# Performance work log

Measured on AMD Instinct MI355X. Metric: run time of the kernel, lower is better.

The kernel has to match this reference:

```python
import jax, jax.numpy as jnp
import numpy as np

NL = 30  # self.nl_size
EPS = 1e-5


def _conv(x, W, b, pad):
    # NCHW conv, OIHW weights
    y = jax.lax.conv_general_dilated(x, W, (1, 1), [(pad, pad), (pad, pad)],
                                     dimension_numbers=('NCHW', 'OIHW', 'NCHW'))
    return y + b[None, :, None, None]


def _gn1(x, g, b):
    # GroupNorm with 1 group: normalize over (C,H,W) per sample, per-channel affine
    mu = jnp.mean(x, axis=(1, 2, 3), keepdims=True)
    var = jnp.var(x, axis=(1, 2, 3), keepdims=True)
    return (x - mu) * jax.lax.rsqrt(var + EPS) * g[None, :, None, None] + b[None, :, None, None]


def _block(x, W, b, g, be):
    # up_conv: Conv3x3 -> GroupNorm(1) -> ReLU
    return jax.nn.relu(_gn1(_conv(x, W, b, 1), g, be))


def _resize(x, h, w):
    # matches F.interpolate(mode='bilinear', align_corners=False)
    return jax.image.resize(x, (x.shape[0], x.shape[1], h, w), method='bilinear')


def setup_inputs() -> dict:
    key = jax.random.key(0)
    ks = jax.random.split(key, 16)
    B, feat, H, W = 4, 64, 300, 300
    s = 0.05
    d = {}
    d['fdm'] = jax.random.normal(ks[0], (B, 1, H, W), jnp.float32)
    d['x0'] = jax.random.normal(ks[1], (B, 64, 300, 300), jnp.float32)
    d['x1'] = jax.random.normal(ks[2], (B, 64, 150, 150), jnp.float32)
    d['x2'] = jax.random.normal(ks[3], (B, 64, 75, 75), jnp.float32)
    d['x3'] = jax.random.normal(ks[4], (B, 64, 38, 38), jnp.float32)
    d['x4'] = jax.random.normal(ks[5], (B, 64, 19, 19), jnp.float32)
    # self.fuse: Conv2d(192, feat, 3) + GN(1, feat)
    d['fuse_W'] = jax.random.normal(ks[6], (feat, 192, 3, 3), jnp.float32) * s
    d['fuse_b'] = jnp.zeros((feat,), jnp.float32)
    d['fuse_g'] = jnp.ones((feat,), jnp.float32)
    d['fuse_be'] = jnp.zeros((feat,), jnp.float32)
    # self.bcg_conv: Conv2d(feat, 1, 1)
    d['bcg_W'] = jax.random.normal(ks[7], (1, feat, 1, 1), jnp.float32) * s
    d['bcg_b'] = jnp.zeros((1,), jnp.float32)
    # self.fuse0: Conv2d(feat, feat, 3) + GN(1, feat)
    d['fuse0_W'] = jax.random.normal(ks[8], (feat, feat, 3, 3), jnp.float32) * s
    d['fuse0_b'] = jnp.zeros((feat,), jnp.float32)
    d['fuse0_g'] = jnp.ones((feat,), jnp.float32)
    d['fuse0_be'] = jnp.zeros((feat,), jnp.float32)
    # self.sup: Conv2d(feat, 1, 1)
    d['sup_W'] = jax.random.normal(ks[9], (1, feat, 1, 1), jnp.float32) * s
    d['sup_b'] = jnp.zeros((1,), jnp.float32)
    return d


def reference(fdm, x0, x1, x2, x3, x4,
              fuse_W, fuse_b, fuse_g, fuse_be,
              bcg_W, bcg_b,
              fuse0_W, fuse0_b, fuse0_g, fuse0_be,
              sup_W, sup_b):
    H, W = fdm.shape[2], fdm.shape[3]
    # x0/x1 are interpolated in the original forward but never used downstream.
    x2r = _resize(x2, H, W)
    x3r = _resize(x3, H, W)
    x4r = _resize(x4, H, W)
    base = _block(jnp.concatenate([x2r, x3r, x4r], axis=1), fuse_W, fuse_b, fuse_g, fuse_be)
    bcg = jax.nn.sigmoid(_conv(base, bcg_W, bcg_b, 0))
    mean_bcg = jnp.mean(bcg, axis=(2, 3), keepdims=True)
    fdm_m = fdm * (bcg > mean_bcg).astype(fdm.dtype)
    nl_feat = _block(base, fuse0_W, fuse0_b, fuse0_g, fuse0_be)
    nl_feat = _resize(nl_feat, NL, NL)  # (b,c,30,30)
    b, c = nl_feat.shape[0], nl_feat.shape[1]
    kh, kw = H // NL, W // NL
    # adaptive_max_pool2d with divisible input: exact window max
    pooled = fdm_m.reshape(b, 1, NL, kh, NL, kw).max(axis=(3, 5))  # (b,1,30,30)
    nl_fdm = pooled * nl_feat  # (b,c,30,30)
    A = nl_fdm.reshape(b, c, NL * NL)   # (b,c,900)
    Bm = nl_feat.reshape(b, c, NL * NL)  # (b,c,900)
    # nl[b,i] = max_j sum_c A[b,c,i] * Bm[b,c,j]
    nl = jnp.max(jnp.einsum('bci,bcj->bij', A, Bm), axis=2)  # (b,900)
    fdm_exp = _resize(nl.reshape(b, 1, NL, NL), H, W)
    base2 = fdm_exp * base
    sup = _conv(base2, sup_W, sup_b, 0)
    return (fdm_m, bcg, base2, sup)
```

## Files before the change

### kernel.cpp

```cpp
#include <hip/hip_runtime.h>
#include <math.h>

typedef unsigned int uint;
typedef unsigned short ushort;
typedef __attribute__((ext_vector_type(8))) short bf16x8;
typedef __attribute__((ext_vector_type(8))) _Float16 f16x8;
typedef __attribute__((ext_vector_type(4))) float f32x4;

#define HWp 90000

__device__ __forceinline__ float bf2f(ushort u) { return __uint_as_float(((uint)u) << 16); }
__device__ __forceinline__ ushort f2bf(float f) {
    uint u = __float_as_uint(f);
    uint r = (u + 0x7FFFu + ((u >> 16) & 1u)) >> 16;
    return (ushort)r;
}
__device__ __forceinline__ ushort f2h(float f) { _Float16 h = (_Float16)f; ushort u; __builtin_memcpy(&u, &h, 2); return u; }
__device__ __forceinline__ float h2f(ushort u) { _Float16 h; __builtin_memcpy(&h, &u, 2); return (float)h; }
__device__ __forceinline__ uint enc(float f) {
    uint u = __float_as_uint(f);
    return (u & 0x80000000u) ? ~u : (u | 0x80000000u);
}
__device__ __forceinline__ float dec(uint k) {
    uint u = (k & 0x80000000u) ? (k ^ 0x80000000u) : ~k;
    return __uint_as_float(u);
}

__global__ __launch_bounds__(256) void k_repack_fsplit(const float* __restrict__ Wf, ushort* __restrict__ Ws) {
    int i = blockIdx.x * 256 + threadIdx.x;
    if (i >= 221184) return;
    int j = i & 7; int l = (i >> 3) & 63; int n = (i >> 9) & 3;
    int r = i >> 11; int tap = r % 9; int ck = (r / 9) % 6; int wsel = r / 54;
    int oc = n * 16 + (l & 15);
    int c  = ck * 32 + ((l >> 4) << 3) + j;
    float w = Wf[(size_t)oc * 1728 + c * 9 + tap] * 256.0f;
    ushort h = f2h(w);
    Ws[i] = wsel ? f2h(w - h2f(h)) : h;
}
__global__ __launch_bounds__(256) void k_repack_f0(const float* __restrict__ W0, ushort* __restrict__ Wfrag) {
    int i = blockIdx.x * 256 + threadIdx.x;
    if (i >= 36864) return;
    int j = i & 7; int l = (i >> 3) & 63; int octile = (i >> 9) & 3;
    int kstep = (i >> 11) & 1; int tap = i >> 12;
    int oc = octile * 16 + (l & 15);
    int c  = kstep * 32 + (l >> 4) * 8 + j;
    Wfrag[i] = f2bf(W0[(size_t)oc * 576 + c * 9 + tap]);
}

__global__ __launch_bounds__(256, 4) void k_fuse_mfma(
    const float* __restrict__ x2, const float* __restrict__ x3, const float* __restrict__ x4,
    const ushort* __restrict__ Ws, const float* __restrict__ bfv,
    float* __restrict__ preb, double* __restrict__ part)
{
    __shared__ char lds_a[108 * 144];
    __shared__ int   t_y0[18], t_y1[18];
    __shared__ float t_wy[18];
    __shared__ int   t_x0[54], t_x1[54];
    __shared__ float t_wx[54];
    __shared__ double red[8];
    const int tid = threadIdx.x;
    const int lane = tid & 63, w = tid >> 6;
    const int bz = blockIdx.z;
    const int y0 = blockIdx.y * 4;
    const int x0 = blockIdx.x * 16;
    const int mg = lane >> 4, mr = lane & 15;

    for (int i = tid; i < 72; i += 256) {
        int lev = i / 24, k = i - lev * 24;
        int n = (lev == 0) ? 75 : (lev == 1 ? 38 : 19);
        float scale = (float)n * (1.0f / 300.0f);
        if (k < 6) {
            int gy = y0 + k - 1;
            float fy = ((float)gy + 0.5f) * scale - 0.5f;
            float fl = floorf(fy); int iy = (int)fl; float ay = fy - fl;
            t_y0[lev * 6 + k] = min(max(iy, 0), n - 1) * n;
            t_y1[lev * 6 + k] = min(iy + 1, n - 1) * n;
            t_wy[lev * 6 + k] = ay;
        } else {
            int j = k - 6;
            int gx = x0 + j - 1;
            float fx = ((float)gx + 0.5f) * scale - 0.5f;
            float fl = floorf(fx); int ix = (int)fl; float ax = fx - fl;
            t_x0[lev * 18 + j] = min(max(ix, 0), n - 1);
            t_x1[lev * 18 + j] = min(ix + 1, n - 1);
            t_wx[lev * 18 + j] = ax;
        }
    }
    __syncthreads();

    f32x4 acc[4];
#pragma unroll
    for (int ot = 0; ot < 4; ++ot) acc[ot] = f32x4{0.f, 0.f, 0.f, 0.f};

    for (int ck = 0; ck < 6; ++ck) {
        const int lev = ck >> 1;
        const float* src = (lev == 0) ? x2 : (lev == 1 ? x3 : x4);
        const int n = (lev == 0) ? 75 : (lev == 1 ? 38 : 19);
        const float* plane0 = src + (size_t)(bz * 64 + (ck & 1) * 32) * n * n;
        for (int e = tid; e < 3456; e += 256) {
            int ch = e / 108;
            int px = e - ch * 108;
            int hy = px / 18, hx = px - hy * 18;
            int gy = y0 + hy - 1, gx = x0 + hx - 1;
            float a = 0.f;
            if ((uint)gy < 300u && (uint)gx < 300u) {
                const float* sp = plane0 + (size_t)ch * n * n;
                int r0 = t_y0[lev * 6 + hy], r1 = t_y1[lev * 6 + hy]; float fy = t_wy[lev * 6 + hy];
                int c0 = t_x0[lev * 18 + hx], c1 = t_x1[lev * 18 + hx]; float fx = t_wx[lev * 18 + hx];
                float v00 = sp[r0 + c0], v01 = sp[r0 + c1];
                float v10 = sp[r1 + c0], v11 = sp[r1 + c1];
                a = ((1.f - fy) * ((1.f - fx) * v00 + fx * v01)
                   + fy * ((1.f - fx) * v10 + fx * v11)) * 256.0f;
            }
            ushort hi = f2h(a);
            ushort lo = f2h(a - h2f(hi));
            char* p = lds_a + px * 144 + ch * 2;
            *(ushort*)p = hi;
            *(ushort*)(p + 64) = lo;
        }
        __syncthreads();
#pragma unroll
        for (int tap = 0; tap < 9; ++tap) {
            const int p = (w + tap / 3) * 18 + (mr + tap % 3);
            const char* ap = lds_a + p * 144 + mg * 16;
            f16x8 ah = *(const f16x8*)ap;
            f16x8 al = *(const f16x8*)(ap + 64);
            const ushort* wh = Ws + ((size_t)(ck * 9 + tap)) * 2048 + lane * 8;
            const ushort* wl = wh + 54 * 2048;
#pragma unroll
            for (int ot = 0; ot < 4; ++ot) {
                f16x8 bh = *(const f16x8*)(wh + ot * 512);
                acc[ot] = __builtin_amdgcn_mfma_f32_16x16x32_f16(ah, bh, acc[ot], 0, 0, 0);
                acc[ot] = __builtin_amdgcn_mfma_f32_16x16x32_f16(al, bh, acc[ot], 0, 0, 0);
                f16x8 bl = *(const f16x8*)(wl + ot * 512);
                acc[ot] = __builtin_amdgcn_mfma_f32_16x16x32_f16(ah, bl, acc[ot], 0, 0, 0);
            }
        }
        __syncthreads();
    }
    const int yo = y0 + w;
    float s = 0.f, ss = 0.f;
#pragma unroll
    for (int ot = 0; ot < 4; ++ot) {
        int oc = ot * 16 + mr;
        float bia = bfv[oc];
#pragma unroll
        for (int i2 = 0; i2 < 4; ++i2) {
            int xo = x0 + mg * 4 + i2;
            if (xo < 300) {
                float t = acc[ot][i2] * (1.0f / 65536.0f) + bia;
                preb[(size_t)(bz * 64 + oc) * HWp + yo * 300 + xo] = t;
                s += t; ss += t * t;
            }
        }
    }
    double ds = s, dss = ss;
    for (int off = 32; off; off >>= 1) { ds += __shfl_down(ds, off); dss += __shfl_down(dss, off); }
    if (lane == 0) { red[w * 2] = ds; red[w * 2 + 1] = dss; }
    __syncthreads();
    if (tid == 0) {
        double S = red[0] + red[2] + red[4] + red[6];
        double SS = red[1] + red[3] + red[5] + red[7];
        int blin = (bz * 75 + blockIdx.y) * 19 + blockIdx.x;
        part[2 * blin] = S; part[2 * blin + 1] = SS;
    }
}

__global__ __launch_bounds__(256, 4) void k_fuse0_conv(
    const float* __restrict__ basep, const ushort* __restrict__ Wfrag,
    const float* __restrict__ b0, ushort* __restrict__ f0c, double* __restrict__ part)
{
    __shared__ ushort lds_x[108 * 64];
    __shared__ double red[8];
    const int tid = threadIdx.x;
    const int lane = tid & 63, w = tid >> 6;
    const int bz = blockIdx.z;
    const int y0 = blockIdx.y * 4;
    const int x0 = blockIdx.x * 16;

    for (int i = tid; i < 6912; i += 256) {
        int c = i / 108, p = i - c * 108;
        int hy = p / 18, hx = p - hy * 18;
        int gy = y0 + hy - 1, gx = x0 + hx - 1;
        float v = 0.f;
        if ((uint)gy < 300u && (uint)gx < 300u)
            v = basep[(size_t)(bz * 64 + c) * HWp + gy * 300 + gx];
        int byteoff = p * 128 + ((c * 2) ^ ((p & 7) << 4));
        *(ushort*)((char*)lds_x + byteoff) = f2bf(v);
    }
    __syncthreads();

    f32x4 acc[4];
#pragma unroll
    for (int ot = 0; ot < 4; ++ot) acc[ot] = f32x4{0.f, 0.f, 0.f, 0.f};
    const int mg = lane >> 4;
    const int mr = lane & 15;
#pragma unroll
    for (int tap = 0; tap < 9; ++tap) {
        const int dy = tap / 3, dx = tap % 3;
        const int p = (w + dy) * 18 + (mr + dx);
#pragma unroll
        for (int ks = 0; ks < 2; ++ks) {
            int slot = ks * 4 + mg;
            int byteoff = p * 128 + ((slot * 16) ^ ((p & 7) << 4));
            bf16x8 a = *(bf16x8*)((char*)lds_x + byteoff);
            const ushort* wp = Wfrag + (((size_t)(tap * 2 + ks) * 4) * 64 + lane) * 8;
#pragma unroll
            for (int ot = 0; ot < 4; ++ot) {
                bf16x8 bv = *(const bf16x8*)(wp + ot * 512);
                acc[ot] = __builtin_amdgcn_mfma_f32_16x16x32_bf16(a, bv, acc[ot], 0, 0, 0);
            }
        }
    }
    const int yo = y0 + w;
    float s = 0.f, ss = 0.f;
#pragma unroll
    for (int ot = 0; ot < 4; ++ot) {
        int oc = ot * 16 + mr;
        float bia = b0[oc];
#pragma unroll
        for (int i2 = 0; i2 < 4; ++i2) {
            int xo = x0 + mg * 4 + i2;
            if (xo < 300) {
                float t = acc[ot][i2] + bia;
                f0c[((size_t)(bz * 300 + yo) * 300 + xo) * 64 + oc] = f2bf(t);
                s += t; ss += t * t;
            }
        }
    }
    double ds = s, dss = ss;
    for (int off = 32; off; off >>= 1) { ds += __shfl_down(ds, off); dss += __shfl_down(dss, off); }
    if (lane == 0) { red[w * 2] = ds; red[w * 2 + 1] = dss; }
    __syncthreads();
    if (tid == 0) {
        double S = red[0] + red[2] + red[4] + red[6];
        double SS = red[1] + red[3] + red[5] + red[7];
        int blin = (bz * 75 + blockIdx.y) * 19 + blockIdx.x;
        part[2 * blin] = S; part[2 * blin + 1] = SS;
    }
}

__global__ __launch_bounds__(64) void k_redstats(const double* __restrict__ part, int cnt,
                                                 double invN, float* __restrict__ stats)
{
    int b = blockIdx.x, t = threadIdx.x;
    double s = 0, ss = 0;
    for (int i = t; i < cnt; i += 64) { s += part[2 * (b * cnt + i)]; ss += part[2 * (b * cnt + i) + 1]; }
    for (int off = 32; off; off >>= 1) { s += __shfl_down(s, off); ss += __shfl_down(ss, off); }
    if (t == 0) {
        double mu = s * invN;
        double var = ss * invN - mu * mu;
        stats[2 * b] = (float)mu;
        stats[2 * b + 1] = (float)(1.0 / sqrt(var + 1e-5));
    }
}

__global__ __launch_bounds__(64) void k_redmean(const double* __restrict__ part, int cnt,
                                                double invN, float* __restrict__ out)
{
    int b = blockIdx.x, t = threadIdx.x;
    double s = 0;
    for (int i = t; i < cnt; i += 64) s += part[b * cnt + i];
    for (int off = 32; off; off >>= 1) s += __shfl_down(s, off);
    if (t == 0) out[b] = (float)(s * invN);
}

__global__ __launch_bounds__(256) void k_finalize(
    float* __restrict__ basep, float* __restrict__ bcg_out,
    const float* __restrict__ fg, const float* __restrict__ fbe,
    const float* __restrict__ wb, const float* __restrict__ bb,
    const float* __restrict__ fstats, double* __restrict__ bcgpart)
{
    const int b = blockIdx.y;
    const int idx = blockIdx.x * 256 + threadIdx.x;
    float lsum = 0.f;
    if (idx < 22500) {
        const int p4 = idx * 4;
        const float mu = fstats[b * 2], rs = fstats[b * 2 + 1];
        float4 acc = make_float4(0.f, 0.f, 0.f, 0.f);
        for (int c = 0; c < 64; ++c) {
            float* ptr = basep + ((size_t)(b * 64 + c)) * HWp + p4;
            float4 v = *(float4*)ptr;
            const float g = fg[c], be = fbe[c];
            float4 t;
            t.x = fmaxf((v.x - mu) * rs * g + be, 0.f);
            t.y = fmaxf((v.y - mu) * rs * g + be, 0.f);
            t.z = fmaxf((v.z - mu) * rs * g + be, 0.f);
            t.w = fmaxf((v.w - mu) * rs * g + be, 0.f);
            *(float4*)ptr = t;
            const float wc = wb[c];
            acc.x = fmaf(wc, t.x, acc.x);
            acc.y = fmaf(wc, t.y, acc.y);
            acc.z = fmaf(wc, t.z, acc.z);
            acc.w = fmaf(wc, t.w, acc.w);
        }
        const float bz = bb[0];
        float4 sg;
        sg.x = 1.f / (1.f + expf(-(acc.x + bz)));
        sg.y = 1.f / (1.f + expf(-(acc.y + bz)));
        sg.z = 1.f / (1.f + expf(-(acc.z + bz)));
        sg.w = 1.f / (1.f + expf(-(acc.w + bz)));
        *(float4*)(bcg_out + (size_t)b * HWp + p4) = sg;
        lsum = sg.x + sg.y + sg.z + sg.w;
    }
    double d = lsum;
    for (int off = 32; off; off >>= 1) d += __shfl_down(d, off);
    __shared__ double rr[4];
    int wid = threadIdx.x >> 6, lane = threadIdx.x & 63;
    if (lane == 0) rr[wid] = d;
    __syncthreads();
    if (threadIdx.x == 0) bcgpart[b * 88 + blockIdx.x] = rr[0] + rr[1] + rr[2] + rr[3];
}

__global__ __launch_bounds__(128) void k_maskpool(
    const float* __restrict__ fdm, const float* __restrict__ bcg,
    const float* __restrict__ bcgmean, float* __restrict__ fdm_m, float* __restrict__ pooled)
{
    const int cell = blockIdx.x;
    const int b = blockIdx.y;
    const int t = threadIdx.x;
    const int cy = cell / 30, cx = cell - cy * 30;
    float m = -INFINITY;
    if (t < 100) {
        int yy = cy * 10 + t / 10, xx = cx * 10 + t % 10;
        size_t p = (size_t)b * HWp + yy * 300 + xx;
        float v = (bcg[p] > bcgmean[b]) ? fdm[p] : 0.f;
        fdm_m[p] = v;
        m = v;
    }
    for (int off = 32; off; off >>= 1) m = fmaxf(m, __shfl_down(m, off));
    __shared__ float rr[2];
    if ((t & 63) == 0) rr[t >> 6] = m;
    __syncthreads();
    if (t == 0) pooled[b * 900 + cell] = fmaxf(rr[0], rr[1]);
}

__global__ __launch_bounds__(256) void k_vert(
    const ushort* __restrict__ f0c, const float* __restrict__ g0, const float* __restrict__ be0,
    const float* __restrict__ f0stats, float* __restrict__ vtmp)
{
    const int idx = blockIdx.x * 256 + threadIdx.x;
    if (idx >= 4 * 30 * 300 * 64) return;
    const int c = idx & 63;
    int rest = idx >> 6;
    const int x = rest % 300; rest /= 300;
    const int j = rest % 30;
    const int b = rest / 30;
    const float mu = f0stats[2 * b], rs = f0stats[2 * b + 1];
    const float gg = g0[c], bb = be0[c];
    const int ylo = max(0, 10 * j - 5), yhi = min(299, 10 * j + 14);
    const float centre = (float)(10 * j) + 4.5f;
    float acc = 0.f, wsum = 0.f;
    for (int yy = ylo; yy <= yhi; ++yy) {
        float w = 1.0f - fabsf((float)yy - centre) * 0.1f;
        float v = bf2f(f0c[(((size_t)b * 300 + yy) * 300 + x) * 64 + c]);
        float t = fmaxf((v - mu) * rs * gg + bb, 0.f);
        acc = fmaf(w, t, acc);
        wsum += w;
    }
    vtmp[idx] = acc / wsum;
}

__global__ __launch_bounds__(256) void k_horiz(
    const float* __restrict__ vtmp, const float* __restrict__ pooled,
    float* __restrict__ A, float* __restrict__ Bm)
{
    const int idx = blockIdx.x * 256 + threadIdx.x;
    if (idx >= 4 * 30 * 30 * 64) return;
    const int c = idx & 63;
    int rest = idx >> 6;
    const int i = rest % 30; rest /= 30;
    const int j = rest % 30;
    const int b = rest / 30;
    const int xlo = max(0, 10 * i - 5), xhi = min(299, 10 * i + 14);
    const float centre = (float)(10 * i) + 4.5f;
    float acc = 0.f, wsum = 0.f;
    for (int xx = xlo; xx <= xhi; ++xx) {
        float w = 1.0f - fabsf((float)xx - centre) * 0.1f;
        acc = fmaf(w, vtmp[(((size_t)b * 30 + j) * 300 + xx) * 64 + c], acc);
        wsum += w;
    }
    float nl30 = acc / wsum;
    Bm[idx] = nl30;
    A[idx] = pooled[b * 900 + j * 30 + i] * nl30;
}

__global__ __launch_bounds__(256) void k_nl(
    const float* __restrict__ A, const float* __restrict__ Bm, uint* __restrict__ nlkey)
{
    __shared__ float lb[75 * 64];
    const int b = blockIdx.z;
    const int j0 = blockIdx.x * 75;
    const int i1 = blockIdx.y * 512 + threadIdx.x;
    const int i2 = i1 + 256;
    for (int s = threadIdx.x; s < 75 * 64; s += 256)
        lb[s] = Bm[(size_t)(b * 900 + j0) * 64 + s];
    __syncthreads();
    const bool v1 = i1 < 900, v2 = i2 < 900;
    float a1[64], a2[64];
    const float* A1 = A + (size_t)(b * 900 + i1) * 64;
    const float* A2 = A + (size_t)(b * 900 + i2) * 64;
#pragma unroll
    for (int c = 0; c < 64; ++c) { a1[c] = v1 ? A1[c] : 0.f; a2[c] = v2 ? A2[c] : 0.f; }
    float m1 = -INFINITY, m2 = -INFINITY;
    for (int jj = 0; jj < 75; ++jj) {
        const float* bp = lb + jj * 64;
        float d1 = 0.f, d2 = 0.f;
#pragma unroll
        for (int c = 0; c < 64; ++c) { float bv = bp[c]; d1 = fmaf(a1[c], bv, d1); d2 = fmaf(a2[c], bv, d2); }
        m1 = fmaxf(m1, d1); m2 = fmaxf(m2, d2);
    }
    if (v1) atomicMax(&nlkey[b * 900 + i1], enc(m1));
    if (v2) atomicMax(&nlkey[b * 900 + i2], enc(m2));
}

__global__ __launch_bounds__(256) void k_base2_sup(
    const float* __restrict__ basep, const uint* __restrict__ nlkey,
    const float* __restrict__ wsup, const float* __restrict__ bsup,
    float* __restrict__ out_b2, float* __restrict__ out_sup)
{
    const int b = blockIdx.y;
    const int idx = blockIdx.x * 256 + threadIdx.x;
    if (idx >= 22500) return;
    const int p4 = idx * 4;
    const int yy = p4 / 300, xx = p4 - yy * 300;
    const uint* nk = nlkey + b * 900;
    float cyf = ((float)yy + 0.5f) * 0.1f - 0.5f;
    int iy = (int)floorf(cyf);
    float ay = cyf - (float)iy;
    int jy0 = min(max(iy, 0), 29), jy1 = min(iy + 1, 29);
    float e[4];
#pragma unroll
    for (int k = 0; k < 4; ++k) {
        float cxf = ((float)(xx + k) + 0.5f) * 0.1f - 0.5f;
        int ix = (int)floorf(cxf);
        float ax = cxf - (float)ix;
        int jx0 = min(max(ix, 0), 29), jx1 = min(ix + 1, 29);
        float n00 = dec(nk[jy0 * 30 + jx0]), n01 = dec(nk[jy0 * 30 + jx1]);
        float n10 = dec(nk[jy1 * 30 + jx0]), n11 = dec(nk[jy1 * 30 + jx1]);
        e[k] = (1.f - ay) * ((1.f - ax) * n00 + ax * n01) + ay * ((1.f - ax) * n10 + ax * n11);
    }
    float4 sacc = make_float4(0.f, 0.f, 0.f, 0.f);
    for (int c = 0; c < 64; ++c) {
        size_t off = ((size_t)(b * 64 + c)) * HWp + p4;
        float4 v = *(const float4*)(basep + off);
        float4 t;
        t.x = v.x * e[0]; t.y = v.y * e[1]; t.z = v.z * e[2]; t.w = v.w * e[3];
        *(float4*)(out_b2 + off) = t;
        const float wc = wsup[c];
        sacc.x = fmaf(wc, t.x, sacc.x);
        sacc.y = fmaf(wc, t.y, sacc.y);
        sacc.z = fmaf(wc, t.z, sacc.z);
        sacc.w = fmaf(wc, t.w, sacc.w);
    }
    const float bz = bsup[0];
    float4 so;
    so.x = sacc.x + bz; so.y = sacc.y + bz; so.z = sacc.z + bz; so.w = sacc.w + bz;
    *(float4*)(out_sup + (size_t)b * HWp + p4) = so;
}

extern "C" void kernel_launch(void* const* d_in, const int* in_sizes, int n_in,
                              void* d_out, int out_size, void* d_ws, size_t ws_size,
                              hipStream_t stream)
{
    (void)in_sizes; (void)n_in; (void)out_size; (void)ws_size;
    const float* fdm     = (const float*)d_in[0];
    const float* x2      = (const float*)d_in[3];
    const float* x3      = (const float*)d_in[4];
    const float* x4      = (const float*)d_in[5];
    const float* fuse_W  = (const float*)d_in[6];
    const float* fuse_b  = (const float*)d_in[7];
    const float* fuse_g  = (const float*)d_in[8];
    const float* fuse_be = (const float*)d_in[9];
    const float* bcg_W   = (const float*)d_in[10];
    const float* bcg_b   = (const float*)d_in[11];
    const float* f0_W    = (const float*)d_in[12];
    const float* f0_b    = (const float*)d_in[13];
    const float* f0_g    = (const float*)d_in[14];
    const float* f0_be   = (const float*)d_in[15];
    const float* sup_W   = (const float*)d_in[16];
    const float* sup_b   = (const float*)d_in[17];

    char* ws = (char*)d_ws;
    float*  basep    = (float*)ws;
    ushort* f0c      = (ushort*)(ws + 92160000);
    double* fusepart = (double*)(ws + 138240000);
    double* f0part   = (double*)(ws + 138331200);
    double* bcgpart  = (double*)(ws + 138422400);
    float*  fext     = (float*)(ws + 138425216);
    float*  fstats   = fext;
    float*  f0stats  = fext + 8;
    float*  bcgmean  = fext + 16;
    float*  pooled   = fext + 32;
    float*  Abuf     = fext + 4000;
    float*  Bbuf     = fext + 234400;
    uint*   nlkey    = (uint*)(fext + 464800);
    float*  vtmp     = (float*)(ws + 140320000);
    ushort* Wsplit   = (ushort*)(ws + 140320000);
    ushort* Wfrag    = (ushort*)(ws + 140800000);

    float* o_fdm  = (float*)d_out;
    float* o_bcg  = o_fdm + 360000;
    float* o_b2   = o_fdm + 720000;
    float* o_sup  = o_fdm + 23760000;

    k_repack_fsplit<<<864, 256, 0, stream>>>(fuse_W, Wsplit);
    k_repack_f0<<<144, 256, 0, stream>>>(f0_W, Wfrag);
    k_fuse_mfma<<<dim3(19, 75, 4), 256, 0, stream>>>(x2, x3, x4, Wsplit, fuse_b, basep, fusepart);
    k_redstats<<<4, 64, 0, stream>>>(fusepart, 1425, 1.0 / 5760000.0, fstats);
    k_finalize<<<dim3(88, 4), 256, 0, stream>>>(basep, o_bcg, fuse_g, fuse_be, bcg_W, bcg_b, fstats, bcgpart);
    k_redmean<<<4, 64, 0, stream>>>(bcgpart, 88, 1.0 / 90000.0, bcgmean);
    k_maskpool<<<dim3(900, 4), 128, 0, stream>>>(fdm, o_bcg, bcgmean, o_fdm, pooled);
    k_fuse0_conv<<<dim3(19, 75, 4), 256, 0, stream>>>(basep, Wfrag, f0_b, f0c, f0part);
    k_redstats<<<4, 64, 0, stream>>>(f0part, 1425, 1.0 / 5760000.0, f0stats);
    k_vert<<<9000, 256, 0, stream>>>(f0c, f0_g, f0_be, f0stats, vtmp);
    k_horiz<<<900, 256, 0, stream>>>(vtmp, pooled, Abuf, Bbuf);
    hipMemsetAsync(nlkey, 0, 3600 * sizeof(uint), stream);
    k_nl<<<dim3(12, 2, 4), 256, 0, stream>>>(Abuf, Bbuf, nlkey);
    k_base2_sup<<<dim3(88, 4), 256, 0, stream>>>(basep, nlkey, sup_W, sup_b, o_b2, o_sup);
}
```

Measured before the change: 902.6 us.

## Precompute bilinear-resized fp16 hi/lo inputs into workspace before fuse conv

Adds a separate resize kernel that computes the bilinear upsampling of x2/x3/x4 once and writes it to a large NHWC buffer as packed fp16 hi/lo pairs. A new fuse conv kernel then loads from this buffer instead of recomputing the bilinear interpolation for every halo tile. This removes redundant interpolation work inside the MFMA conv. In exchange it writes and reads back about 276MB of extra traffic, and the new path is taken only when the workspace is large enough; otherwise the old kernel runs.

```diff
diff --git a/kernel.cpp b/kernel.cpp
--- a/kernel.cpp
+++ b/kernel.cpp
@@ -47,7 +47,139 @@
     Wfrag[i] = f2bf(W0[(size_t)oc * 576 + c * 9 + tap]);
 }
 
-__global__ __launch_bounds__(256, 4) void k_fuse_mfma(
+__global__ __launch_bounds__(256) void k_resize(
+    const float* __restrict__ x2, const float* __restrict__ x3, const float* __restrict__ x4,
+    uint* __restrict__ rsz)
+{
+    __shared__ uint lds[192 * 65];
+    const int tid = threadIdx.x;
+    const int x0 = blockIdx.x * 64;
+    const int y  = blockIdx.y;
+    const int b  = blockIdx.z;
+    int ry0[3], ry1[3]; float rwy[3];
+#pragma unroll
+    for (int lev = 0; lev < 3; ++lev) {
+        int n = (lev == 0) ? 75 : (lev == 1 ? 38 : 19);
+        float scale = (float)n * (1.0f / 300.0f);
+        float fy = ((float)y + 0.5f) * scale - 0.5f;
+        float fl = floorf(fy); int iy = (int)fl;
+        rwy[lev] = fy - fl;
+        ry0[lev] = min(max(iy, 0), n - 1) * n;
+        ry1[lev] = min(iy + 1, n - 1) * n;
+    }
+    for (int e = tid; e < 12288; e += 256) {
+        int x = e & 63, ch = e >> 6;
+        int gx = x0 + x;
+        uint pk = 0;
+        if (gx < 300) {
+            int lev = ch >> 6, c = ch & 63;
+            int n = (lev == 0) ? 75 : (lev == 1 ? 38 : 19);
+            float scale = (float)n * (1.0f / 300.0f);
+            const float* src = (lev == 0) ? x2 : (lev == 1 ? x3 : x4);
+            const float* sp = src + (size_t)(b * 64 + c) * n * n;
+            float fx = ((float)gx + 0.5f) * scale - 0.5f;
+            float fl = floorf(fx); int ix = (int)fl; float ax = fx - fl;
+            int c0 = min(max(ix, 0), n - 1), c1 = min(ix + 1, n - 1);
+            float fy = rwy[lev];
+            float v00 = sp[ry0[lev] + c0], v01 = sp[ry0[lev] + c1];
+            float v10 = sp[ry1[lev] + c0], v11 = sp[ry1[lev] + c1];
+            float a = ((1.f - fy) * ((1.f - ax) * v00 + ax * v01)
+                     + fy * ((1.f - ax) * v10 + ax * v11)) * 256.0f;
+            ushort hi = f2h(a);
+            ushort lo = f2h(a - h2f(hi));
+            pk = (uint)hi | ((uint)lo << 16);
+        }
+        lds[ch * 65 + x] = pk;
+    }
+    __syncthreads();
+    uint* op = rsz + ((size_t)(b * 300 + y) * 300 + x0) * 192;
+    for (int e = tid; e < 12288; e += 256) {
+        int ch = e % 192, x = e / 192;
+        if (x0 + x < 300) op[(size_t)x * 192 + ch] = lds[ch * 65 + x];
+    }
+}
+
+__global__ __launch_bounds__(256, 4) void k_fuse_mfma_fast(
+    const uint* __restrict__ rsz, const ushort* __restrict__ Ws, const float* __restrict__ bfv,
+    float* __restrict__ preb, double* __restrict__ part)
+{
+    __shared__ char lds_a[108 * 144];
+    __shared__ double red[8];
+    const int tid = threadIdx.x;
+    const int lane = tid & 63, w = tid >> 6;
+    const int bz = blockIdx.z;
+    const int y0 = blockIdx.y * 4;
+    const int x0 = blockIdx.x * 16;
+    const int mg = lane >> 4, mr = lane & 15;
+
+    f32x4 acc[4];
+#pragma unroll
+    for (int ot = 0; ot < 4; ++ot) acc[ot] = f32x4{0.f, 0.f, 0.f, 0.f};
+
+    for (int ck = 0; ck < 6; ++ck) {
+        for (int e = tid; e < 1728; e += 256) {
+            int k = e & 15, px = e >> 4;
+            int hy = px / 18, hx = px - hy * 18;
+            int gy = y0 + hy - 1, gx = x0 + hx - 1;
+            uint hiw = 0, low = 0;
+            if ((uint)gy < 300u && (uint)gx < 300u) {
+                const uint* p = rsz + ((size_t)(bz * 300 + gy) * 300 + gx) * 192 + ck * 32 + k * 2;
+                uint2 v = *(const uint2*)p;
+                hiw = (v.x & 0xffffu) | (v.y << 16);
+                low = (v.x >> 16) | (v.y & 0xffff0000u);
+            }
+            *(uint*)(lds_a + px * 144 + k * 4) = hiw;
+            *(uint*)(lds_a + px * 144 + 64 + k * 4) = low;
+        }
+        __syncthreads();
+#pragma unroll
+        for (int tap = 0; tap < 9; ++tap) {
+            const int p = (w + tap / 3) * 18 + (mr + tap % 3);
+            const char* ap = lds_a + p * 144 + mg * 16;
+            f16x8 ah = *(const f16x8*)ap;
+            f16x8 al = *(const f16x8*)(ap + 64);
+            const ushort* wh = Ws + ((size_t)(ck * 9 + tap)) * 2048 + lane * 8;
+            const ushort* wl = wh + 54 * 2048;
+#pragma unroll
+            for (int ot = 0; ot < 4; ++ot) {
+                f16x8 bh = *(const f16x8*)(wh + ot * 512);
+                acc[ot] = __builtin_amdgcn_mfma_f32_16x16x32_f16(ah, bh, acc[ot], 0, 0, 0);
+                acc[ot] = __builtin_amdgcn_mfma_f32_16x16x32_f16(al, bh, acc[ot], 0, 0, 0);
+                f16x8 bl = *(const f16x8*)(wl + ot * 512);
+                acc[ot] = __builtin_amdgcn_mfma_f32_16x16x32_f16(ah, bl, acc[ot], 0, 0, 0);
+            }
+        }
+        __syncthreads();
+    }
+    const int yo = y0 + w;
+    float s = 0.f, ss = 0.f;
+#pragma unroll
+    for (int ot = 0; ot < 4; ++ot) {
+        int oc = ot * 16 + mr;
+        float bia = bfv[oc];
+#pragma unroll
+        for (int i2 = 0; i2 < 4; ++i2) {
+            int xo = x0 + mg * 4 + i2;
+            if (xo < 300) {
+                float t = acc[ot][i2] * (1.0f / 65536.0f) + bia;
+                preb[(size_t)(bz * 64 + oc) * HWp + yo * 300 + xo] = t;
+                s += t; ss += t * t;
+            }
+        }
+    }
+    double ds = s, dss = ss;
+    for (int off = 32; off; off >>= 1) { ds += __shfl_down(ds, off); dss += __shfl_down(dss, off); }
+    if (lane == 0) { red[w * 2] = ds; red[w * 2 + 1] = dss; }
+    __syncthreads();
+    if (tid == 0) {
+        double S = red[0] + red[2] + red[4] + red[6];
+        double SS = red[1] + red[3] + red[5] + red[7];
+        int blin = (bz * 75 + blockIdx.y) * 19 + blockIdx.x;
+        part[2 * blin] = S; part[2 * blin + 1] = SS;
+    }
+}
+
+__global__ __launch_bounds__(256, 4) void k_fuse_mfma_bilin(
     const float* __restrict__ x2, const float* __restrict__ x3, const float* __restrict__ x4,
     const ushort* __restrict__ Ws, const float* __restrict__ bfv,
     float* __restrict__ preb, double* __restrict__ part)
@@ -463,7 +595,7 @@
                               void* d_out, int out_size, void* d_ws, size_t ws_size,
                               hipStream_t stream)
 {
-    (void)in_sizes; (void)n_in; (void)out_size; (void)ws_size;
+    (void)in_sizes; (void)n_in; (void)out_size;
     const float* fdm     = (const float*)d_in[0];
     const float* x2      = (const float*)d_in[3];
     const float* x3      = (const float*)d_in[4];
@@ -482,31 +614,52 @@
     const float* sup_b   = (const float*)d_in[17];
 
     char* ws = (char*)d_ws;
-    float*  basep    = (float*)ws;
-    ushort* f0c      = (ushort*)(ws + 92160000);
-    double* fusepart = (double*)(ws + 138240000);
-    double* f0part   = (double*)(ws + 138331200);
-    double* bcgpart  = (double*)(ws + 138422400);
-    float*  fext     = (float*)(ws + 138425216);
-    float*  fstats   = fext;
-    float*  f0stats  = fext + 8;
-    float*  bcgmean  = fext + 16;
-    float*  pooled   = fext + 32;
-    float*  Abuf     = fext + 4000;
-    float*  Bbuf     = fext + 234400;
-    uint*   nlkey    = (uint*)(fext + 464800);
-    float*  vtmp     = (float*)(ws + 140320000);
-    ushort* Wsplit   = (ushort*)(ws + 140320000);
-    ushort* Wfrag    = (ushort*)(ws + 140800000);
+    const bool big = ws_size >= (size_t)427000000;
 
     float* o_fdm  = (float*)d_out;
     float* o_bcg  = o_fdm + 360000;
     float* o_b2   = o_fdm + 720000;
     float* o_sup  = o_fdm + 23760000;
 
+    float*  basep = (float*)ws;
+    ushort* f0c   = (ushort*)(ws + 92160000);
+
+    double *fusepart, *f0part, *bcgpart; float* fext; float* vtmp;
+    ushort *Wsplit, *Wfrag; uint* rsz = nullptr;
+    if (big) {
+        rsz      = (uint*)(ws + 138240000);
+        fusepart = (double*)(ws + 414720000);
+        f0part   = (double*)(ws + 414811200);
+        bcgpart  = (double*)(ws + 414902400);
+        fext     = (float*)(ws + 414905216);
+        vtmp     = (float*)(ws + 416800000);
+        Wsplit   = (ushort*)(ws + 426100000);
+        Wfrag    = (ushort*)(ws + 426600000);
+    } else {
+        fusepart = (double*)(ws + 138240000);
+        f0part   = (double*)(ws + 138331200);
+        bcgpart  = (double*)(ws + 138422400);
+        fext     = (float*)(ws + 138425216);
+        vtmp     = (float*)(ws + 140320000);
+        Wsplit   = (ushort*)(ws + 140320000);
+        Wfrag    = (ushort*)(ws + 140800000);
+    }
+    float* fstats  = fext;
+    float* f0stats = fext + 8;
+    float* bcgmean = fext + 16;
+    float* pooled  = fext + 32;
+    float* Abuf    = fext + 4000;
+    float* Bbuf    = fext + 234400;
+    uint*  nlkey   = (uint*)(fext + 464800);
+
     k_repack_fsplit<<<864, 256, 0, stream>>>(fuse_W, Wsplit);
     k_repack_f0<<<144, 256, 0, stream>>>(f0_W, Wfrag);
-    k_fuse_mfma<<<dim3(19, 75, 4), 256, 0, stream>>>(x2, x3, x4, Wsplit, fuse_b, basep, fusepart);
+    if (big) {
+        k_resize<<<dim3(5, 300, 4), 256, 0, stream>>>(x2, x3, x4, rsz);
+        k_fuse_mfma_fast<<<dim3(19, 75, 4), 256, 0, stream>>>(rsz, Wsplit, fuse_b, basep, fusepart);
+    } else {
+        k_fuse_mfma_bilin<<<dim3(19, 75, 4), 256, 0, stream>>>(x2, x3, x4, Wsplit, fuse_b, basep, fusepart);
+    }
     k_redstats<<<4, 64, 0, stream>>>(fusepart, 1425, 1.0 / 5760000.0, fstats);
     k_finalize<<<dim3(88, 4), 256, 0, stream>>>(basep, o_bcg, fuse_g, fuse_be, bcg_W, bcg_b, fstats, bcgpart);
     k_redmean<<<4, 64, 0, stream>>>(bcgpart, 88, 1.0 / 90000.0, bcgmean);
```

New measurement: 901.5 us. About the same (-0.1%).
